# Performance work log

Measured on AMD Instinct MI355X. Metric: run time of the kernel, lower is better.

The kernel has to match this reference:

```python
import jax, jax.numpy as jnp
import numpy as np

DIM = 1024
N_HEADS = 16
HEAD_DIM = DIM // N_HEADS
EPS = 1e-05
ROPE_BASE = 1000000.0


def apply_rope(x, base=ROPE_BASE):
    # x: [b, seq, heads, head_dim]
    b, seq, n_heads, dim = x.shape
    half = dim // 2
    i = jnp.arange(half)
    theta = 1.0 / base ** (2 * i / dim)
    pos = jnp.arange(seq)
    angles = pos[:, None] * theta[None, :]            # [seq, half]
    cos = jnp.cos(angles)[None, :, None, :]           # [1, seq, 1, half]
    sin = jnp.sin(angles)[None, :, None, :]
    x1, x2 = jnp.split(x, 2, axis=-1)
    return jnp.concatenate([x1 * cos - x2 * sin, x1 * sin + x2 * cos], axis=-1)


def setup_inputs() -> dict:
    key = jax.random.key(0)
    ks = jax.random.split(key, 6)
    b, seq = 2, 2048
    scale = 1.0 / np.sqrt(DIM)
    x = jax.random.normal(ks[0], (b, seq, DIM), dtype=jnp.float32)
    w_norm = jnp.ones((DIM,), dtype=jnp.float32)
    Wq = jax.random.normal(ks[1], (DIM, DIM), dtype=jnp.float32) * scale
    Wk = jax.random.normal(ks[2], (DIM, DIM), dtype=jnp.float32) * scale
    Wv = jax.random.normal(ks[3], (DIM, DIM), dtype=jnp.float32) * scale
    Wo = jax.random.normal(ks[4], (DIM, DIM), dtype=jnp.float32) * scale
    return {"x": x, "w_norm": w_norm, "Wq": Wq, "Wk": Wk, "Wv": Wv, "Wo": Wo}


def reference(x, w_norm, Wq, Wk, Wv, Wo):
    b, seq, d = x.shape
    # RMSNorm
    rms = jnp.sqrt(jnp.mean(x * x, axis=-1, keepdims=True) + EPS)
    x_norm = x / rms * w_norm
    # QKV projections (Dense without bias: y = x @ W)
    q = (x_norm @ Wq).reshape(b, seq, N_HEADS, HEAD_DIM)
    k = (x_norm @ Wk).reshape(b, seq, N_HEADS, HEAD_DIM)
    v = (x_norm @ Wv).reshape(b, seq, N_HEADS, HEAD_DIM)
    q = apply_rope(q)
    k = apply_rope(k)
    # Causal attention with full [b,h,t,s] scores (faithful to source)
    scores = jnp.einsum('bthd,bshd->bhts', q, k) / jnp.sqrt(jnp.float32(HEAD_DIM))
    causal = jnp.triu(jnp.full((seq, seq), -jnp.inf, dtype=scores.dtype), k=1)
    scores = scores + causal[None, None, :, :]
    attn = jax.nn.softmax(scores, axis=-1)
    out = jnp.einsum('bhts,bshd->bthd', attn, v).reshape(b, seq, d)
    return out @ Wo
```

## Files before the change

kernel.cpp:

```cpp
#include <hip/hip_runtime.h>

#define DIM 1024
#define SEQ 2048
#define BATCH 2
#define NHEADS 16
#define HD 64
#define ROWS (BATCH * SEQ)

typedef __bf16 bf16x8 __attribute__((ext_vector_type(8)));
typedef __bf16 bf16x4 __attribute__((ext_vector_type(4)));
typedef float f32x4 __attribute__((ext_vector_type(4)));

__device__ __forceinline__ f32x4 f4zero() {
    f32x4 z = {0.f, 0.f, 0.f, 0.f};
    return z;
}

__global__ __launch_bounds__(256) void rmsnorm_bf16(const float* __restrict__ x,
                                                    const float* __restrict__ w,
                                                    __bf16* __restrict__ xn) {
    int row = blockIdx.x;
    int t = threadIdx.x;
    float4 v = ((const float4*)(x + (size_t)row * DIM))[t];
    float ss = v.x * v.x + v.y * v.y + v.z * v.z + v.w * v.w;
#pragma unroll
    for (int off = 1; off < 64; off <<= 1) ss += __shfl_xor(ss, off);
    __shared__ float red[4];
    if ((t & 63) == 0) red[t >> 6] = ss;
    __syncthreads();
    ss = red[0] + red[1] + red[2] + red[3];
    float scale = rsqrtf(ss * (1.0f / DIM) + 1e-5f);
    float4 wv = ((const float4*)w)[t];
    bf16x4 o;
    o[0] = (__bf16)(v.x * scale * wv.x);
    o[1] = (__bf16)(v.y * scale * wv.y);
    o[2] = (__bf16)(v.z * scale * wv.z);
    o[3] = (__bf16)(v.w * scale * wv.w);
    *(bf16x4*)(xn + (size_t)row * DIM + t * 4) = o;
}

__global__ __launch_bounds__(256) void wcvt_kernel(const float* __restrict__ Wq,
                                                   const float* __restrict__ Wk,
                                                   const float* __restrict__ Wv,
                                                   const float* __restrict__ Wo,
                                                   __bf16* tq, __bf16* tk, __bf16* tv, __bf16* to_) {
    int z = blockIdx.z;
    const float* W = z == 0 ? Wq : z == 1 ? Wk : z == 2 ? Wv : Wo;
    __bf16* T = z == 0 ? tq : z == 1 ? tk : z == 2 ? tv : to_;
    __shared__ float tile[32][33];
    int n0 = blockIdx.x * 32, k0 = blockIdx.y * 32;
    int tx = threadIdx.x & 31, ty = threadIdx.x >> 5;
#pragma unroll
    for (int j = 0; j < 32; j += 8) tile[ty + j][tx] = W[(size_t)(k0 + ty + j) * DIM + n0 + tx];
    __syncthreads();
#pragma unroll
    for (int j = 0; j < 32; j += 8)
        T[(size_t)(n0 + ty + j) * DIM + k0 + tx] = (__bf16)tile[tx][ty + j];
}

__global__ __launch_bounds__(256) void rope_table_kernel(float* __restrict__ cosT,
                                                         float* __restrict__ sinT) {
    int idx = blockIdx.x * 256 + threadIdx.x;
    int s = idx >> 5, i = idx & 31;
    float e = (2.0f * (float)i) / 64.0f;
    float theta = 1.0f / powf(1000000.0f, e);
    float ang = (float)s * theta;
    cosT[idx] = cosf(ang);
    sinT[idx] = sinf(ang);
}

__global__ __launch_bounds__(256) void rope_apply_bf16(__bf16* __restrict__ q,
                                                       __bf16* __restrict__ k,
                                                       const float* __restrict__ cosT,
                                                       const float* __restrict__ sinT) {
    int idx = blockIdx.x * 256 + threadIdx.x;
    __bf16* t = blockIdx.y ? k : q;
    int row = idx >> 6, rem = idx & 63;
    int head = rem >> 2, i0 = (rem & 3) * 8;
    int s = row & (SEQ - 1);
    size_t base = (size_t)row * DIM + head * HD + i0;
    bf16x8 x1 = *(const bf16x8*)&t[base];
    bf16x8 x2 = *(const bf16x8*)&t[base + 32];
    const float* cp = cosT + s * 32 + i0;
    const float* sp = sinT + s * 32 + i0;
    bf16x8 y1, y2;
#pragma unroll
    for (int j = 0; j < 8; ++j) {
        float a = (float)x1[j], b = (float)x2[j];
        float c = cp[j], sn = sp[j];
        y1[j] = (__bf16)(a * c - b * sn);
        y2[j] = (__bf16)(a * sn + b * c);
    }
    *(bf16x8*)&t[base] = y1;
    *(bf16x8*)&t[base + 32] = y2;
}

__global__ __launch_bounds__(256) void vtrans_kernel(const __bf16* __restrict__ v,
                                                     __bf16* __restrict__ vt) {
    __shared__ __bf16 tile[32][33];
    int bh = blockIdx.z;
    int b = bh >> 4, h = bh & 15;
    int s0 = blockIdx.x * 32, d0 = blockIdx.y * 32;
    int tx = threadIdx.x & 31, ty = threadIdx.x >> 5;
    const __bf16* src = v + (size_t)(b * SEQ) * DIM + h * HD;
#pragma unroll
    for (int j = 0; j < 32; j += 8) tile[ty + j][tx] = src[(size_t)(s0 + ty + j) * DIM + d0 + tx];
    __syncthreads();
    __bf16* dst = vt + ((size_t)bh * HD + d0) * SEQ + s0;
#pragma unroll
    for (int j = 0; j < 32; j += 8) dst[(size_t)(ty + j) * SEQ + tx] = tile[tx][ty + j];
}

template <typename OutT>
__device__ __forceinline__ void gemm_body(const __bf16* __restrict__ A,
                                          const __bf16* __restrict__ Bt,
                                          OutT* __restrict__ C,
                                          int K, int N, int row0, int col0) {
    __shared__ __bf16 As[128][56];
    __shared__ __bf16 Bs[128][56];
    int tid = threadIdx.x;
    int w = tid >> 6, l = tid & 63, l15 = l & 15, g = l >> 4;
    int wr = (w >> 1) << 6, wc = (w & 1) << 6;
    int c0 = tid, c1 = tid + 256;
    int r0 = c0 >> 2, o0 = (c0 & 3) * 8;
    int r1 = c1 >> 2, o1 = (c1 & 3) * 8;

    f32x4 acc[4][4];
#pragma unroll
    for (int i = 0; i < 4; ++i)
#pragma unroll
        for (int j = 0; j < 4; ++j) acc[i][j] = f4zero();

    bf16x8 ra[2], rb[2];
    ra[0] = *(const bf16x8*)&A[(size_t)(row0 + r0) * K + o0];
    ra[1] = *(const bf16x8*)&A[(size_t)(row0 + r1) * K + o1];
    rb[0] = *(const bf16x8*)&Bt[(size_t)(col0 + r0) * K + o0];
    rb[1] = *(const bf16x8*)&Bt[(size_t)(col0 + r1) * K + o1];

    for (int k0 = 0; k0 < K; k0 += 32) {
        __syncthreads();
        *(bf16x8*)&As[r0][o0] = ra[0];
        *(bf16x8*)&As[r1][o1] = ra[1];
        *(bf16x8*)&Bs[r0][o0] = rb[0];
        *(bf16x8*)&Bs[r1][o1] = rb[1];
        __syncthreads();
        if (k0 + 32 < K) {
            int kn = k0 + 32;
            ra[0] = *(const bf16x8*)&A[(size_t)(row0 + r0) * K + kn + o0];
            ra[1] = *(const bf16x8*)&A[(size_t)(row0 + r1) * K + kn + o1];
            rb[0] = *(const bf16x8*)&Bt[(size_t)(col0 + r0) * K + kn + o0];
            rb[1] = *(const bf16x8*)&Bt[(size_t)(col0 + r1) * K + kn + o1];
        }
        bf16x8 af[4], bfr[4];
#pragma unroll
        for (int i = 0; i < 4; ++i) af[i] = *(const bf16x8*)&As[wr + i * 16 + l15][g * 8];
#pragma unroll
        for (int j = 0; j < 4; ++j) bfr[j] = *(const bf16x8*)&Bs[wc + j * 16 + l15][g * 8];
#pragma unroll
        for (int i = 0; i < 4; ++i)
#pragma unroll
            for (int j = 0; j < 4; ++j)
                acc[i][j] = __builtin_amdgcn_mfma_f32_16x16x32_bf16(af[i], bfr[j], acc[i][j], 0, 0, 0);
    }
#pragma unroll
    for (int i = 0; i < 4; ++i)
#pragma unroll
        for (int j = 0; j < 4; ++j)
#pragma unroll
            for (int r = 0; r < 4; ++r) {
                int row = row0 + wr + i * 16 + g * 4 + r;
                int col = col0 + wc + j * 16 + l15;
                C[(size_t)row * N + col] = (OutT)acc[i][j][r];
            }
}

__global__ __launch_bounds__(256) void gemm_qkv_kernel(const __bf16* __restrict__ xn,
                                                       const __bf16* __restrict__ wq,
                                                       const __bf16* __restrict__ wk,
                                                       const __bf16* __restrict__ wv,
                                                       __bf16* q, __bf16* k, __bf16* v) {
    int z = blockIdx.z;
    const __bf16* Bt = z == 0 ? wq : z == 1 ? wk : wv;
    __bf16* C = z == 0 ? q : z == 1 ? k : v;
    gemm_body<__bf16>(xn, Bt, C, DIM, DIM, (int)blockIdx.y << 7, (int)blockIdx.x << 7);
}

__global__ __launch_bounds__(256) void gemm_out_kernel(const __bf16* __restrict__ ctx,
                                                       const __bf16* __restrict__ wo,
                                                       float* __restrict__ out) {
    gemm_body<float>(ctx, wo, out, DIM, DIM, (int)blockIdx.y << 7, (int)blockIdx.x << 7);
}

__global__ __launch_bounds__(256) void attn_mfma_kernel(const __bf16* __restrict__ q,
                                                        const __bf16* __restrict__ k,
                                                        const __bf16* __restrict__ vt,
                                                        __bf16* __restrict__ ctx) {
    int bh = blockIdx.x;
    int qt = 31 - (int)blockIdx.y;
    int b = bh >> 4, h = bh & 15;
    int q0 = qt << 6;
    __shared__ __bf16 Ks[64][72];
    __shared__ __bf16 Vl[64][72];
    __shared__ __bf16 Ps[4][16][72];
    int tid = threadIdx.x, w = tid >> 6, l = tid & 63, l15 = l & 15, g = l >> 4;
    size_t hoff = (size_t)(b * SEQ) * DIM + h * HD;
    const __bf16* vth = vt + (size_t)bh * HD * SEQ;

    bf16x8 aq[2];
    {
        int qrow = q0 + w * 16 + l15;
        aq[0] = *(const bf16x8*)&q[hoff + (size_t)qrow * DIM + g * 8];
        aq[1] = *(const bf16x8*)&q[hoff + (size_t)qrow * DIM + 32 + g * 8];
    }

    f32x4 acc_o[4];
#pragma unroll
    for (int j = 0; j < 4; ++j) acc_o[j] = f4zero();
    float m_run[4], l_run[4];
#pragma unroll
    for (int r = 0; r < 4; ++r) {
        m_run[r] = -1e30f;
        l_run[r] = 0.f;
    }

    int c0 = tid, c1 = tid + 256;
    int kr0 = c0 >> 3, ko0 = (c0 & 7) * 8;
    int kr1 = c1 >> 3, ko1 = (c1 & 7) * 8;
    bf16x8 rk[2], rv[2];
    rk[0] = *(const bf16x8*)&k[hoff + (size_t)kr0 * DIM + ko0];
    rk[1] = *(const bf16x8*)&k[hoff + (size_t)kr1 * DIM + ko1];
    rv[0] = *(const bf16x8*)&vth[(size_t)kr0 * SEQ + ko0];
    rv[1] = *(const bf16x8*)&vth[(size_t)kr1 * SEQ + ko1];

    for (int st = 0; st <= qt; ++st) {
        int s0 = st << 6;
        __syncthreads();
        *(bf16x8*)&Ks[kr0][ko0] = rk[0];
        *(bf16x8*)&Ks[kr1][ko1] = rk[1];
        *(bf16x8*)&Vl[kr0][ko0] = rv[0];
        *(bf16x8*)&Vl[kr1][ko1] = rv[1];
        __syncthreads();
        if (st < qt) {
            int sn = s0 + 64;
            rk[0] = *(const bf16x8*)&k[hoff + (size_t)(sn + kr0) * DIM + ko0];
            rk[1] = *(const bf16x8*)&k[hoff + (size_t)(sn + kr1) * DIM + ko1];
            rv[0] = *(const bf16x8*)&vth[(size_t)kr0 * SEQ + sn + ko0];
            rv[1] = *(const bf16x8*)&vth[(size_t)kr1 * SEQ + sn + ko1];
        }

        f32x4 sacc[4];
#pragma unroll
        for (int j = 0; j < 4; ++j) sacc[j] = f4zero();
#pragma unroll
        for (int j = 0; j < 4; ++j) {
            bf16x8 bk0 = *(const bf16x8*)&Ks[j * 16 + l15][g * 8];
            bf16x8 bk1 = *(const bf16x8*)&Ks[j * 16 + l15][32 + g * 8];
            sacc[j] = __builtin_amdgcn_mfma_f32_16x16x32_bf16(aq[0], bk0, sacc[j], 0, 0, 0);
            sacc[j] = __builtin_amdgcn_mfma_f32_16x16x32_bf16(aq[1], bk1, sacc[j], 0, 0, 0);
        }

        bool diag = (st == qt);
#pragma unroll
        for (int r = 0; r < 4; ++r) {
            int rowq = q0 + w * 16 + g * 4 + r;
            float mt = -3e38f;
#pragma unroll
            for (int j = 0; j < 4; ++j) {
                float vsc = sacc[j][r] * 0.125f;
                if (diag && (s0 + j * 16 + l15) > rowq) vsc = -1e30f;
                sacc[j][r] = vsc;
                mt = fmaxf(mt, vsc);
            }
#pragma unroll
            for (int off = 1; off < 16; off <<= 1) mt = fmaxf(mt, __shfl_xor(mt, off));
            float m_new = fmaxf(m_run[r], mt);
            float alpha = __expf(m_run[r] - m_new);
            float rs = 0.f;
#pragma unroll
            for (int j = 0; j < 4; ++j) {
                float p = __expf(sacc[j][r] - m_new);
                sacc[j][r] = p;
                rs += p;
            }
#pragma unroll
            for (int off = 1; off < 16; off <<= 1) rs += __shfl_xor(rs, off);
            l_run[r] = l_run[r] * alpha + rs;
            m_run[r] = m_new;
#pragma unroll
            for (int j = 0; j < 4; ++j) acc_o[j][r] *= alpha;
        }

#pragma unroll
        for (int r = 0; r < 4; ++r)
#pragma unroll
            for (int j = 0; j < 4; ++j) Ps[w][g * 4 + r][j * 16 + l15] = (__bf16)sacc[j][r];

        bf16x8 ap0 = *(const bf16x8*)&Ps[w][l15][g * 8];
        bf16x8 ap1 = *(const bf16x8*)&Ps[w][l15][32 + g * 8];
#pragma unroll
        for (int jd = 0; jd < 4; ++jd) {
            bf16x8 bv0 = *(const bf16x8*)&Vl[jd * 16 + l15][g * 8];
            bf16x8 bv1 = *(const bf16x8*)&Vl[jd * 16 + l15][32 + g * 8];
            acc_o[jd] = __builtin_amdgcn_mfma_f32_16x16x32_bf16(ap0, bv0, acc_o[jd], 0, 0, 0);
            acc_o[jd] = __builtin_amdgcn_mfma_f32_16x16x32_bf16(ap1, bv1, acc_o[jd], 0, 0, 0);
        }
    }

#pragma unroll
    for (int r = 0; r < 4; ++r) {
        float inv = 1.0f / l_run[r];
        int row = q0 + w * 16 + g * 4 + r;
#pragma unroll
        for (int jd = 0; jd < 4; ++jd)
            ctx[hoff + (size_t)row * DIM + jd * 16 + l15] = (__bf16)(acc_o[jd][r] * inv);
    }
}

extern "C" void kernel_launch(void* const* d_in, const int* in_sizes, int n_in,
                              void* d_out, int out_size, void* d_ws, size_t ws_size,
                              hipStream_t stream) {
    const float* x = (const float*)d_in[0];
    const float* w_norm = (const float*)d_in[1];
    const float* Wq = (const float*)d_in[2];
    const float* Wk = (const float*)d_in[3];
    const float* Wv = (const float*)d_in[4];
    const float* Wo = (const float*)d_in[5];
    float* out = (float*)d_out;
    char* w8 = (char*)d_ws;

    __bf16* xn = (__bf16*)(w8);
    __bf16* wtq = (__bf16*)(w8 + (8ull << 20));
    __bf16* wtk = (__bf16*)(w8 + (10ull << 20));
    __bf16* wtv = (__bf16*)(w8 + (12ull << 20));
    __bf16* wto = (__bf16*)(w8 + (14ull << 20));
    __bf16* qb = (__bf16*)(w8 + (16ull << 20));
    __bf16* kb = (__bf16*)(w8 + (24ull << 20));
    __bf16* vb = (__bf16*)(w8 + (32ull << 20));
    __bf16* vtb = (__bf16*)(w8 + (40ull << 20));
    __bf16* ctx = (__bf16*)(w8 + (48ull << 20));
    float* cosT = (float*)(w8 + (56ull << 20));
    float* sinT = cosT + SEQ * 32;

    wcvt_kernel<<<dim3(32, 32, 4), 256, 0, stream>>>(Wq, Wk, Wv, Wo, wtq, wtk, wtv, wto);
    rmsnorm_bf16<<<ROWS, 256, 0, stream>>>(x, w_norm, xn);
    rope_table_kernel<<<(SEQ * 32) / 256, 256, 0, stream>>>(cosT, sinT);

    gemm_qkv_kernel<<<dim3(DIM / 128, ROWS / 128, 3), 256, 0, stream>>>(xn, wtq, wtk, wtv, qb, kb, vb);

    rope_apply_bf16<<<dim3((ROWS * 64) / 256, 2), 256, 0, stream>>>(qb, kb, cosT, sinT);
    vtrans_kernel<<<dim3(SEQ / 32, HD / 32, BATCH * NHEADS), 256, 0, stream>>>(vb, vtb);

    attn_mfma_kernel<<<dim3(BATCH * NHEADS, SEQ / 64), 256, 0, stream>>>(qb, kb, vtb, ctx);

    gemm_out_kernel<<<dim3(DIM / 128, ROWS / 128), 256, 0, stream>>>(ctx, wto, out);
}
```

Measured before the change: 158.6 us.

## Use direct global-to-LDS loads in GEMM and widen attention KV tiles with lazy rescale

```diff
diff --git a/kernel.cpp b/kernel.cpp
--- a/kernel.cpp
+++ b/kernel.cpp
@@ -15,6 +15,10 @@
     f32x4 z = {0.f, 0.f, 0.f, 0.f};
     return z;
 }
+
+#define GLOAD_LDS16(g, l)                                                                  \
+    __builtin_amdgcn_global_load_lds((const __attribute__((address_space(1))) void*)(g),   \
+                                     (__attribute__((address_space(3))) void*)(l), 16, 0, 0)
 
 __global__ __launch_bounds__(256) void rmsnorm_bf16(const float* __restrict__ x,
                                                     const float* __restrict__ w,
@@ -116,51 +120,52 @@
                                           const __bf16* __restrict__ Bt,
                                           OutT* __restrict__ C,
                                           int K, int N, int row0, int col0) {
-    __shared__ __bf16 As[128][56];
-    __shared__ __bf16 Bs[128][56];
+    __shared__ __bf16 As[128 * 32];
+    __shared__ __bf16 Bs[128 * 32];
     int tid = threadIdx.x;
     int w = tid >> 6, l = tid & 63, l15 = l & 15, g = l >> 4;
     int wr = (w >> 1) << 6, wc = (w & 1) << 6;
-    int c0 = tid, c1 = tid + 256;
-    int r0 = c0 >> 2, o0 = (c0 & 3) * 8;
-    int r1 = c1 >> 2, o1 = (c1 & 3) * 8;
+
+    int sr0 = tid >> 2;
+    int sr1 = 64 + (tid >> 2);
+    int lc0 = (((tid & 3) ^ ((tid >> 3) & 3)) << 3);
+    const __bf16* gA0 = A + (size_t)(row0 + sr0) * K + lc0;
+    const __bf16* gA1 = A + (size_t)(row0 + sr1) * K + lc0;
+    const __bf16* gB0 = Bt + (size_t)(col0 + sr0) * K + lc0;
+    const __bf16* gB1 = Bt + (size_t)(col0 + sr1) * K + lc0;
+    __bf16* lA0 = As + w * 512;
+    __bf16* lA1 = As + 2048 + w * 512;
+    __bf16* lB0 = Bs + w * 512;
+    __bf16* lB1 = Bs + 2048 + w * 512;
+
+    int rca = ((g ^ ((l15 >> 1) & 3)) << 3);
 
     f32x4 acc[4][4];
 #pragma unroll
     for (int i = 0; i < 4; ++i)
 #pragma unroll
         for (int j = 0; j < 4; ++j) acc[i][j] = f4zero();
-
-    bf16x8 ra[2], rb[2];
-    ra[0] = *(const bf16x8*)&A[(size_t)(row0 + r0) * K + o0];
-    ra[1] = *(const bf16x8*)&A[(size_t)(row0 + r1) * K + o1];
-    rb[0] = *(const bf16x8*)&Bt[(size_t)(col0 + r0) * K + o0];
-    rb[1] = *(const bf16x8*)&Bt[(size_t)(col0 + r1) * K + o1];
 
     for (int k0 = 0; k0 < K; k0 += 32) {
         __syncthreads();
-        *(bf16x8*)&As[r0][o0] = ra[0];
-        *(bf16x8*)&As[r1][o1] = ra[1];
-        *(bf16x8*)&Bs[r0][o0] = rb[0];
-        *(bf16x8*)&Bs[r1][o1] = rb[1];
+        GLOAD_LDS16(gA0 + k0, lA0);
+        GLOAD_LDS16(gA1 + k0, lA1);
+        GLOAD_LDS16(gB0 + k0, lB0);
+        GLOAD_LDS16(gB1 + k0, lB1);
         __syncthreads();
-        if (k0 + 32 < K) {
-            int kn = k0 + 32;
-            ra[0] = *(const bf16x8*)&A[(size_t)(row0 + r0) * K + kn + o0];
-            ra[1] = *(const bf16x8*)&A[(size_t)(row0 + r1) * K + kn + o1];
-            rb[0] = *(const bf16x8*)&Bt[(size_t)(col0 + r0) * K + kn + o0];
-            rb[1] = *(const bf16x8*)&Bt[(size_t)(col0 + r1) * K + kn + o1];
-        }
+
         bf16x8 af[4], bfr[4];
 #pragma unroll
-        for (int i = 0; i < 4; ++i) af[i] = *(const bf16x8*)&As[wr + i * 16 + l15][g * 8];
-#pragma unroll
-        for (int j = 0; j < 4; ++j) bfr[j] = *(const bf16x8*)&Bs[wc + j * 16 + l15][g * 8];
+        for (int i = 0; i < 4; ++i) af[i] = *(const bf16x8*)&As[(wr + i * 16 + l15) * 32 + rca];
+#pragma unroll
+        for (int j = 0; j < 4; ++j) bfr[j] = *(const bf16x8*)&Bs[(wc + j * 16 + l15) * 32 + rca];
+        __builtin_amdgcn_s_setprio(1);
 #pragma unroll
         for (int i = 0; i < 4; ++i)
 #pragma unroll
             for (int j = 0; j < 4; ++j)
                 acc[i][j] = __builtin_amdgcn_mfma_f32_16x16x32_bf16(af[i], bfr[j], acc[i][j], 0, 0, 0);
+        __builtin_amdgcn_s_setprio(0);
     }
 #pragma unroll
     for (int i = 0; i < 4; ++i)
@@ -199,9 +204,9 @@
     int qt = 31 - (int)blockIdx.y;
     int b = bh >> 4, h = bh & 15;
     int q0 = qt << 6;
-    __shared__ __bf16 Ks[64][72];
-    __shared__ __bf16 Vl[64][72];
-    __shared__ __bf16 Ps[4][16][72];
+    __shared__ __bf16 Ks[128][72];
+    __shared__ __bf16 Vl[64][136];
+    __shared__ __bf16 Ps[4][16][136];
     int tid = threadIdx.x, w = tid >> 6, l = tid & 63, l15 = l & 15, g = l >> 4;
     size_t hoff = (size_t)(b * SEQ) * DIM + h * HD;
     const __bf16* vth = vt + (size_t)bh * HD * SEQ;
@@ -209,8 +214,14 @@
     bf16x8 aq[2];
     {
         int qrow = q0 + w * 16 + l15;
-        aq[0] = *(const bf16x8*)&q[hoff + (size_t)qrow * DIM + g * 8];
-        aq[1] = *(const bf16x8*)&q[hoff + (size_t)qrow * DIM + 32 + g * 8];
+        bf16x8 t0 = *(const bf16x8*)&q[hoff + (size_t)qrow * DIM + g * 8];
+        bf16x8 t1 = *(const bf16x8*)&q[hoff + (size_t)qrow * DIM + 32 + g * 8];
+        const float c2 = 0.125f * 1.44269504f;
+#pragma unroll
+        for (int j = 0; j < 8; ++j) {
+            aq[0][j] = (__bf16)((float)t0[j] * c2);
+            aq[1][j] = (__bf16)((float)t1[j] * c2);
+        }
     }
 
     f32x4 acc_o[4];
@@ -223,87 +234,99 @@
         l_run[r] = 0.f;
     }
 
-    int c0 = tid, c1 = tid + 256;
-    int kr0 = c0 >> 3, ko0 = (c0 & 7) * 8;
-    int kr1 = c1 >> 3, ko1 = (c1 & 7) * 8;
-    bf16x8 rk[2], rv[2];
-    rk[0] = *(const bf16x8*)&k[hoff + (size_t)kr0 * DIM + ko0];
-    rk[1] = *(const bf16x8*)&k[hoff + (size_t)kr1 * DIM + ko1];
-    rv[0] = *(const bf16x8*)&vth[(size_t)kr0 * SEQ + ko0];
-    rv[1] = *(const bf16x8*)&vth[(size_t)kr1 * SEQ + ko1];
-
-    for (int st = 0; st <= qt; ++st) {
-        int s0 = st << 6;
+    int ksr = tid >> 3, kd0 = (tid & 7) * 8;
+    int vdr = tid >> 4, vs0 = (tid & 15) * 8;
+
+    int nst = (q0 + 191) >> 7;
+    bf16x8 rk[4], rv[4];
+#pragma unroll
+    for (int c = 0; c < 4; ++c) {
+        rk[c] = *(const bf16x8*)&k[hoff + (size_t)(c * 32 + ksr) * DIM + kd0];
+        rv[c] = *(const bf16x8*)&vth[(size_t)(c * 16 + vdr) * SEQ + vs0];
+    }
+
+    for (int st = 0; st < nst; ++st) {
+        int s0 = st << 7;
         __syncthreads();
-        *(bf16x8*)&Ks[kr0][ko0] = rk[0];
-        *(bf16x8*)&Ks[kr1][ko1] = rk[1];
-        *(bf16x8*)&Vl[kr0][ko0] = rv[0];
-        *(bf16x8*)&Vl[kr1][ko1] = rv[1];
+#pragma unroll
+        for (int c = 0; c < 4; ++c) {
+            *(bf16x8*)&Ks[c * 32 + ksr][kd0] = rk[c];
+            *(bf16x8*)&Vl[c * 16 + vdr][vs0] = rv[c];
+        }
         __syncthreads();
-        if (st < qt) {
-            int sn = s0 + 64;
-            rk[0] = *(const bf16x8*)&k[hoff + (size_t)(sn + kr0) * DIM + ko0];
-            rk[1] = *(const bf16x8*)&k[hoff + (size_t)(sn + kr1) * DIM + ko1];
-            rv[0] = *(const bf16x8*)&vth[(size_t)kr0 * SEQ + sn + ko0];
-            rv[1] = *(const bf16x8*)&vth[(size_t)kr1 * SEQ + sn + ko1];
-        }
-
-        f32x4 sacc[4];
-#pragma unroll
-        for (int j = 0; j < 4; ++j) sacc[j] = f4zero();
-#pragma unroll
-        for (int j = 0; j < 4; ++j) {
+        if (st + 1 < nst) {
+            int sn = s0 + 128;
+#pragma unroll
+            for (int c = 0; c < 4; ++c) {
+                rk[c] = *(const bf16x8*)&k[hoff + (size_t)(sn + c * 32 + ksr) * DIM + kd0];
+                rv[c] = *(const bf16x8*)&vth[(size_t)(c * 16 + vdr) * SEQ + sn + vs0];
+            }
+        }
+
+        f32x4 sacc[8];
+#pragma unroll
+        for (int j = 0; j < 8; ++j) sacc[j] = f4zero();
+        __builtin_amdgcn_s_setprio(1);
+#pragma unroll
+        for (int j = 0; j < 8; ++j) {
             bf16x8 bk0 = *(const bf16x8*)&Ks[j * 16 + l15][g * 8];
             bf16x8 bk1 = *(const bf16x8*)&Ks[j * 16 + l15][32 + g * 8];
             sacc[j] = __builtin_amdgcn_mfma_f32_16x16x32_bf16(aq[0], bk0, sacc[j], 0, 0, 0);
             sacc[j] = __builtin_amdgcn_mfma_f32_16x16x32_bf16(aq[1], bk1, sacc[j], 0, 0, 0);
         }
-
-        bool diag = (st == qt);
+        __builtin_amdgcn_s_setprio(0);
+
+        if (st == nst - 1) {
+#pragma unroll
+            for (int j = 0; j < 8; ++j) {
+                int scol = s0 + j * 16 + l15;
+#pragma unroll
+                for (int r = 0; r < 4; ++r) {
+                    int rowq = q0 + w * 16 + g * 4 + r;
+                    if (scol > rowq) sacc[j][r] = -1e30f;
+                }
+            }
+        }
+
 #pragma unroll
         for (int r = 0; r < 4; ++r) {
-            int rowq = q0 + w * 16 + g * 4 + r;
-            float mt = -3e38f;
-#pragma unroll
-            for (int j = 0; j < 4; ++j) {
-                float vsc = sacc[j][r] * 0.125f;
-                if (diag && (s0 + j * 16 + l15) > rowq) vsc = -1e30f;
-                sacc[j][r] = vsc;
-                mt = fmaxf(mt, vsc);
-            }
-#pragma unroll
-            for (int off = 1; off < 16; off <<= 1) mt = fmaxf(mt, __shfl_xor(mt, off));
-            float m_new = fmaxf(m_run[r], mt);
-            float alpha = __expf(m_run[r] - m_new);
+            float tl = sacc[0][r];
+#pragma unroll
+            for (int j = 1; j < 8; ++j) tl = fmaxf(tl, sacc[j][r]);
+            if (!__all(tl <= m_run[r] + 11.0f)) {
+#pragma unroll
+                for (int off = 1; off < 16; off <<= 1) tl = fmaxf(tl, __shfl_xor(tl, off));
+                float m_new = fmaxf(m_run[r], tl);
+                float alpha = exp2f(m_run[r] - m_new);
+                l_run[r] *= alpha;
+#pragma unroll
+                for (int jd = 0; jd < 4; ++jd) acc_o[jd][r] *= alpha;
+                m_run[r] = m_new;
+            }
             float rs = 0.f;
 #pragma unroll
-            for (int j = 0; j < 4; ++j) {
-                float p = __expf(sacc[j][r] - m_new);
-                sacc[j][r] = p;
+            for (int j = 0; j < 8; ++j) {
+                float p = exp2f(sacc[j][r] - m_run[r]);
+                Ps[w][g * 4 + r][j * 16 + l15] = (__bf16)p;
                 rs += p;
             }
 #pragma unroll
             for (int off = 1; off < 16; off <<= 1) rs += __shfl_xor(rs, off);
-            l_run[r] = l_run[r] * alpha + rs;
-            m_run[r] = m_new;
-#pragma unroll
-            for (int j = 0; j < 4; ++j) acc_o[j][r] *= alpha;
-        }
-
-#pragma unroll
-        for (int r = 0; r < 4; ++r)
-#pragma unroll
-            for (int j = 0; j < 4; ++j) Ps[w][g * 4 + r][j * 16 + l15] = (__bf16)sacc[j][r];
-
-        bf16x8 ap0 = *(const bf16x8*)&Ps[w][l15][g * 8];
-        bf16x8 ap1 = *(const bf16x8*)&Ps[w][l15][32 + g * 8];
-#pragma unroll
-        for (int jd = 0; jd < 4; ++jd) {
-            bf16x8 bv0 = *(const bf16x8*)&Vl[jd * 16 + l15][g * 8];
-            bf16x8 bv1 = *(const bf16x8*)&Vl[jd * 16 + l15][32 + g * 8];
-            acc_o[jd] = __builtin_amdgcn_mfma_f32_16x16x32_bf16(ap0, bv0, acc_o[jd], 0, 0, 0);
-            acc_o[jd] = __builtin_amdgcn_mfma_f32_16x16x32_bf16(ap1, bv1, acc_o[jd], 0, 0, 0);
-        }
+            l_run[r] += rs;
+        }
+
+        bf16x8 ap[4];
+#pragma unroll
+        for (int ks = 0; ks < 4; ++ks) ap[ks] = *(const bf16x8*)&Ps[w][l15][ks * 32 + g * 8];
+        __builtin_amdgcn_s_setprio(1);
+#pragma unroll
+        for (int jd = 0; jd < 4; ++jd)
+#pragma unroll
+            for (int ks = 0; ks < 4; ++ks) {
+                bf16x8 bv = *(const bf16x8*)&Vl[jd * 16 + l15][ks * 32 + g * 8];
+                acc_o[jd] = __builtin_amdgcn_mfma_f32_16x16x32_bf16(ap[ks], bv, acc_o[jd], 0, 0, 0);
+            }
+        __builtin_amdgcn_s_setprio(0);
     }
 
 #pragma unroll
```

New measurement: 149.5 us. 1.06x faster.
